# Optimization experiments

Measured on AMD Instinct MI355X. Metric: run time of the kernel, lower is better.

Reference implementation:

```python
import jax, jax.numpy as jnp
import numpy as np

B, S, D_MODEL, D_K, D_V = 4, 2048, 1024, 1024, 1024


def setup_inputs() -> dict:
    key = jax.random.key(0)
    k1, k2, k3, k4 = jax.random.split(key, 4)
    scale = 1.0 / np.sqrt(D_MODEL)
    x = jax.random.normal(k1, (B, S, D_MODEL), dtype=jnp.float32)
    Wq = jax.random.normal(k2, (D_K, D_MODEL), dtype=jnp.float32) * scale
    Wk = jax.random.normal(k3, (D_K, D_MODEL), dtype=jnp.float32) * scale
    Wv = jax.random.normal(k4, (D_V, D_MODEL), dtype=jnp.float32) * scale
    # causal mask: position i may attend to j <= i (True = keep)
    mask = jnp.broadcast_to(jnp.tril(jnp.ones((S, S), dtype=bool)), (B, S, S))
    return {"x": x, "mask": mask, "Wq": Wq, "Wk": Wk, "Wv": Wv}


def reference(x, mask, Wq, Wk, Wv):
    # nn.Linear(d, k, bias=False): y = x @ W.T with W of shape [k, d]
    q = jnp.einsum('bsd,kd->bsk', x, Wq)
    k = jnp.einsum('bsd,kd->bsk', x, Wk)
    v = jnp.einsum('bsd,vd->bsv', x, Wv)
    scores = jnp.einsum('bik,bjk->bij', q, k) / jnp.sqrt(jnp.float32(D_K))
    s = jnp.where(mask, scores, -jnp.inf)
    # masked, fully-masked-row-safe softmax (fully masked rows -> all zeros,
    # matching softmax[all-masked rows] = 0 in the original)
    m = jnp.max(s, axis=-1, keepdims=True)
    m_safe = jnp.where(jnp.isfinite(m), m, 0.0)
    e = jnp.exp(s - m_safe)          # exp(-inf) = 0 for masked entries
    denom = jnp.sum(e, axis=-1, keepdims=True)
    p = e / jnp.where(denom == 0.0, 1.0, denom)
    return jnp.einsum('bij,bjv->biv', p, v)
```

## Files before the change

kernel.cpp:

```cpp
#include <hip/hip_runtime.h>
#include <hip/hip_bf16.h>
#include <stdint.h>

#define SEQ   2048
#define DM    1024
#define NBAT  4

typedef __attribute__((ext_vector_type(8))) short  short8;
typedef __attribute__((ext_vector_type(4))) float  floatx4;

__device__ __forceinline__ unsigned short f2b(float f) {
    __hip_bfloat16 h = __float2bfloat16(f);
    unsigned short r;
    __builtin_memcpy(&r, &h, 2);
    return r;
}

__device__ __forceinline__ void gload16(const void* g, void* s) {
    __builtin_amdgcn_global_load_lds(
        (const __attribute__((address_space(1))) unsigned int*)(uintptr_t)g,
        (__attribute__((address_space(3))) unsigned int*)(uintptr_t)s,
        16, 0, 0);
}

__global__ void cast_bf16_4(const float4* __restrict__ in, ushort4* __restrict__ out, int n4) {
    int i = blockIdx.x * 256 + threadIdx.x;
    if (i < n4) {
        float4 f = in[i];
        ushort4 u;
        u.x = f2b(f.x); u.y = f2b(f.y); u.z = f2b(f.z); u.w = f2b(f.w);
        out[i] = u;
    }
}

template<int OUTM, bool TRI, bool KLIM, bool REV>
__global__ __launch_bounds__(256) void gemm_bt(
    const unsigned short* __restrict__ A, const unsigned short* __restrict__ Bm,
    void* __restrict__ Cv,
    unsigned short* __restrict__ Qo, unsigned short* __restrict__ Ko,
    unsigned short* __restrict__ Vto,
    int M, int N, int K,
    long long sA, long long sB, long long sC, float qscale)
{
    int m0, n0;
    if (TRI) {
        const int f = blockIdx.x;
        int ti = (int)((sqrtf(8.f * f + 1.f) - 1.f) * 0.5f);
        if ((ti + 1) * (ti + 2) / 2 <= f) ti++;
        if (ti * (ti + 1) / 2 > f) ti--;
        const int tj = f - ti * (ti + 1) / 2;
        m0 = ti * 128;
        n0 = tj * 128;
    } else {
        m0 = (REV ? (gridDim.y - 1 - blockIdx.y) : blockIdx.y) * 128;
        n0 = blockIdx.x * 128;
    }
    const int z = blockIdx.z;
    A  += (size_t)z * sA;
    Bm += (size_t)z * sB;

    __shared__ __align__(16) unsigned short As[128 * 32];
    __shared__ __align__(16) unsigned short Bs[128 * 32];

    const int t    = threadIdx.x;
    const int w    = t >> 6;
    const int lane = t & 63;
    const int wr   = w >> 1, wc = w & 1;
    const int r    = lane & 15, q = lane >> 4;

    floatx4 acc[4][4];
#pragma unroll
    for (int i = 0; i < 4; i++)
#pragma unroll
        for (int j = 0; j < 4; j++)
            acc[i][j] = (floatx4){0.f, 0.f, 0.f, 0.f};

    const int kEnd = KLIM ? ((m0 + 128 < K) ? m0 + 128 : K) : K;

    const int row0 = t >> 2;
    const int cc0  = t & 3;

    for (int k0 = 0; k0 < kEnd; k0 += 32) {
        const size_t ka = (size_t)k0 + cc0 * 8;
        gload16(A  + (size_t)(m0 + row0)      * K + ka, As + (size_t)w * 512);
        gload16(A  + (size_t)(m0 + row0 + 64) * K + ka, As + 2048 + (size_t)w * 512);
        gload16(Bm + (size_t)(n0 + row0)      * K + ka, Bs + (size_t)w * 512);
        gload16(Bm + (size_t)(n0 + row0 + 64) * K + ka, Bs + 2048 + (size_t)w * 512);
        __builtin_amdgcn_s_waitcnt(0);
        __syncthreads();

        short8 af[4], bf[4];
#pragma unroll
        for (int i = 0; i < 4; i++) {
            af[i] = *(const short8*)&As[(wr * 64 + i * 16 + r) * 32 + q * 8];
            bf[i] = *(const short8*)&Bs[(wc * 64 + i * 16 + r) * 32 + q * 8];
        }
#pragma unroll
        for (int i = 0; i < 4; i++)
#pragma unroll
            for (int j = 0; j < 4; j++)
                acc[i][j] = __builtin_amdgcn_mfma_f32_16x16x32_bf16(af[i], bf[j], acc[i][j], 0, 0, 0);
        __syncthreads();
    }

    const int gmb = m0 + wr * 64 + q * 4;
    const int gnb = n0 + wc * 64 + r;
    if (OUTM == 2) {
        float* C = (float*)Cv + (size_t)z * sC;
#pragma unroll
        for (int i = 0; i < 4; i++)
#pragma unroll
            for (int j = 0; j < 4; j++) {
                const int gm = gmb + i * 16;
                const int gn = gnb + j * 16;
#pragma unroll
                for (int rr = 0; rr < 4; rr++)
                    C[(size_t)(gm + rr) * N + gn] = acc[i][j][rr];
            }
    } else {
#pragma unroll
        for (int i = 0; i < 4; i++) {
            const int gm = gmb + i * 16;
#pragma unroll
            for (int j = 0; j < 4; j++) {
                const int gn = gnb + j * 16;
                if (n0 < 1024) {
#pragma unroll
                    for (int rr = 0; rr < 4; rr++)
                        Qo[(size_t)(gm + rr) * 1024 + gn] = f2b(acc[i][j][rr] * qscale);
                } else if (n0 < 2048) {
#pragma unroll
                    for (int rr = 0; rr < 4; rr++)
                        Ko[(size_t)(gm + rr) * 1024 + (gn - 1024)] = f2b(acc[i][j][rr]);
                } else {
                    const int b = gm >> 11;
                    const int s = gm & 2047;
                    const int v = gn - 2048;
                    ushort4 u;
                    u.x = f2b(acc[i][j][0]);
                    u.y = f2b(acc[i][j][1]);
                    u.z = f2b(acc[i][j][2]);
                    u.w = f2b(acc[i][j][3]);
                    *(ushort4*)&Vto[((size_t)(b * 1024 + v)) * 2048 + s] = u;
                }
            }
        }
    }
}

__global__ __launch_bounds__(256) void softmax_causal(const float* __restrict__ Sc,
                                                      unsigned short* __restrict__ P)
{
    const int i = blockIdx.x;
    const int b = blockIdx.y;
    const float* row = Sc + ((size_t)b * SEQ + i) * SEQ;
    unsigned short* prow = P + ((size_t)b * SEQ + i) * SEQ;
    const int nv = i + 1;
    const int t = threadIdx.x;

    float v[8];
    float mx = -1e30f;
#pragma unroll
    for (int jj = 0; jj < 8; jj++) {
        const int j = t + jj * 256;
        const float x = (j < nv) ? row[j] : -1e30f;
        v[jj] = x;
        mx = fmaxf(mx, x);
    }
#pragma unroll
    for (int off = 32; off >= 1; off >>= 1)
        mx = fmaxf(mx, __shfl_xor(mx, off, 64));
    __shared__ float redmx[4];
    __shared__ float redsm[4];
    if ((t & 63) == 0) redmx[t >> 6] = mx;
    __syncthreads();
    mx = fmaxf(fmaxf(redmx[0], redmx[1]), fmaxf(redmx[2], redmx[3]));

    float e[8];
    float sum = 0.f;
#pragma unroll
    for (int jj = 0; jj < 8; jj++) {
        const int j = t + jj * 256;
        e[jj] = (j < nv) ? __expf(v[jj] - mx) : 0.f;
        sum += e[jj];
    }
#pragma unroll
    for (int off = 32; off >= 1; off >>= 1)
        sum += __shfl_xor(sum, off, 64);
    if ((t & 63) == 0) redsm[t >> 6] = sum;
    __syncthreads();
    sum = redsm[0] + redsm[1] + redsm[2] + redsm[3];

    const float inv = 1.f / sum;
#pragma unroll
    for (int jj = 0; jj < 8; jj++) {
        const int j = t + jj * 256;
        prow[j] = f2b(e[jj] * inv);
    }
}

extern "C" void kernel_launch(void* const* d_in, const int* in_sizes, int n_in,
                              void* d_out, int out_size, void* d_ws, size_t ws_size,
                              hipStream_t stream) {
    (void)in_sizes; (void)n_in; (void)out_size; (void)ws_size;
    const float* x  = (const float*)d_in[0];
    const float* Wq = (const float*)d_in[2];
    const float* Wk = (const float*)d_in[3];
    const float* Wv = (const float*)d_in[4];

    char* base = (char*)d_ws;
    size_t off = 0;
    auto alloc = [&](size_t n) { char* p = base + off; off += (n + 255) & ~(size_t)255; return p; };

    unsigned short* xb   = (unsigned short*)alloc((size_t)NBAT * SEQ * DM * 2);
    unsigned short* wall = (unsigned short*)alloc((size_t)3 * DM * DM * 2);
    unsigned short* Qb   = (unsigned short*)alloc((size_t)NBAT * SEQ * DM * 2);
    unsigned short* Kb   = (unsigned short*)alloc((size_t)NBAT * SEQ * DM * 2);
    unsigned short* Vtb  = (unsigned short*)alloc((size_t)NBAT * DM * SEQ * 2);
    float*          Sc   = (float*)alloc((size_t)NBAT * SEQ * SEQ * 4);
    unsigned short* P    = (unsigned short*)alloc((size_t)NBAT * SEQ * SEQ * 2);

    const dim3 blk(256);

    {
        int n4 = NBAT * SEQ * DM / 4;
        cast_bf16_4<<<dim3((n4 + 255) / 256), blk, 0, stream>>>((const float4*)x, (ushort4*)xb, n4);
        int w4 = DM * DM / 4;
        dim3 wg((w4 + 255) / 256);
        cast_bf16_4<<<wg, blk, 0, stream>>>((const float4*)Wq, (ushort4*)(wall),            w4);
        cast_bf16_4<<<wg, blk, 0, stream>>>((const float4*)Wk, (ushort4*)(wall + DM * DM),  w4);
        cast_bf16_4<<<wg, blk, 0, stream>>>((const float4*)Wv, (ushort4*)(wall + 2 * DM * DM), w4);
    }

    const int Mtot = NBAT * SEQ;

    gemm_bt<3, false, false, false><<<dim3(3 * DM / 128, Mtot / 128, 1), blk, 0, stream>>>(
        xb, wall, nullptr, Qb, Kb, Vtb, Mtot, 3 * DM, DM, 0, 0, 0, 0.03125f);

    gemm_bt<2, true, false, false><<<dim3(136, 1, NBAT), blk, 0, stream>>>(
        Qb, Kb, Sc, nullptr, nullptr, nullptr, SEQ, SEQ, DM,
        (long long)SEQ * DM, (long long)SEQ * DM, (long long)SEQ * SEQ, 1.0f);

    softmax_causal<<<dim3(SEQ, NBAT), blk, 0, stream>>>(Sc, P);

    gemm_bt<2, false, true, true><<<dim3(DM / 128, SEQ / 128, NBAT), blk, 0, stream>>>(
        P, Vtb, d_out, nullptr, nullptr, nullptr, SEQ, DM, SEQ,
        (long long)SEQ * SEQ, (long long)DM * SEQ, (long long)SEQ * DM, 1.0f);
}
```

Before: 317.2 us.

## Fuse causal softmax into QK^T epilogue and defer normalization to PV GEMM

The fp32 score matrix and the separate softmax kernel are removed. The QK^T GEMM epilogue now applies the causal mask, computes exp directly, writes bf16 unnormalized probabilities, and atomically accumulates per-row sums into a zeroed buffer. The PV GEMM epilogue divides each output row by its row sum. This removes a large fp32 write and read plus a kernel launch. In exchange it drops the max subtraction, so exp can overflow if scores are large, and it adds atomics on the row sums.

```diff
diff --git a/kernel.cpp b/kernel.cpp
--- a/kernel.cpp
+++ b/kernel.cpp
@@ -33,12 +33,18 @@
     }
 }
 
+__global__ void zero_f32(float* __restrict__ p, int n) {
+    int i = blockIdx.x * 256 + threadIdx.x;
+    if (i < n) p[i] = 0.f;
+}
+
 template<int OUTM, bool TRI, bool KLIM, bool REV>
 __global__ __launch_bounds__(256) void gemm_bt(
     const unsigned short* __restrict__ A, const unsigned short* __restrict__ Bm,
     void* __restrict__ Cv,
     unsigned short* __restrict__ Qo, unsigned short* __restrict__ Ko,
     unsigned short* __restrict__ Vto,
+    float* __restrict__ rowsum,
     int M, int N, int K,
     long long sA, long long sB, long long sC, float qscale)
 {
@@ -105,19 +111,7 @@
 
     const int gmb = m0 + wr * 64 + q * 4;
     const int gnb = n0 + wc * 64 + r;
-    if (OUTM == 2) {
-        float* C = (float*)Cv + (size_t)z * sC;
-#pragma unroll
-        for (int i = 0; i < 4; i++)
-#pragma unroll
-            for (int j = 0; j < 4; j++) {
-                const int gm = gmb + i * 16;
-                const int gn = gnb + j * 16;
-#pragma unroll
-                for (int rr = 0; rr < 4; rr++)
-                    C[(size_t)(gm + rr) * N + gn] = acc[i][j][rr];
-            }
-    } else {
+    if (OUTM == 3) {
 #pragma unroll
         for (int i = 0; i < 4; i++) {
             const int gm = gmb + i * 16;
@@ -145,57 +139,44 @@
                 }
             }
         }
-    }
-}
-
-__global__ __launch_bounds__(256) void softmax_causal(const float* __restrict__ Sc,
-                                                      unsigned short* __restrict__ P)
-{
-    const int i = blockIdx.x;
-    const int b = blockIdx.y;
-    const float* row = Sc + ((size_t)b * SEQ + i) * SEQ;
-    unsigned short* prow = P + ((size_t)b * SEQ + i) * SEQ;
-    const int nv = i + 1;
-    const int t = threadIdx.x;
-
-    float v[8];
-    float mx = -1e30f;
-#pragma unroll
-    for (int jj = 0; jj < 8; jj++) {
-        const int j = t + jj * 256;
-        const float x = (j < nv) ? row[j] : -1e30f;
-        v[jj] = x;
-        mx = fmaxf(mx, x);
-    }
-#pragma unroll
-    for (int off = 32; off >= 1; off >>= 1)
-        mx = fmaxf(mx, __shfl_xor(mx, off, 64));
-    __shared__ float redmx[4];
-    __shared__ float redsm[4];
-    if ((t & 63) == 0) redmx[t >> 6] = mx;
-    __syncthreads();
-    mx = fmaxf(fmaxf(redmx[0], redmx[1]), fmaxf(redmx[2], redmx[3]));
-
-    float e[8];
-    float sum = 0.f;
-#pragma unroll
-    for (int jj = 0; jj < 8; jj++) {
-        const int j = t + jj * 256;
-        e[jj] = (j < nv) ? __expf(v[jj] - mx) : 0.f;
-        sum += e[jj];
-    }
-#pragma unroll
-    for (int off = 32; off >= 1; off >>= 1)
-        sum += __shfl_xor(sum, off, 64);
-    if ((t & 63) == 0) redsm[t >> 6] = sum;
-    __syncthreads();
-    sum = redsm[0] + redsm[1] + redsm[2] + redsm[3];
-
-    const float inv = 1.f / sum;
-#pragma unroll
-    for (int jj = 0; jj < 8; jj++) {
-        const int j = t + jj * 256;
-        prow[j] = f2b(e[jj] * inv);
+    } else if (OUTM == 4) {
+        unsigned short* E = (unsigned short*)Cv + (size_t)z * sC;
+        float* rs = rowsum + (size_t)z * SEQ;
+#pragma unroll
+        for (int i = 0; i < 4; i++) {
+            const int gm = gmb + i * 16;
+#pragma unroll
+            for (int rr = 0; rr < 4; rr++) {
+                float part = 0.f;
+#pragma unroll
+                for (int j = 0; j < 4; j++) {
+                    const int gn = gnb + j * 16;
+                    const float ev = (gn <= gm + rr) ? __expf(acc[i][j][rr]) : 0.f;
+                    part += ev;
+                    E[(size_t)(gm + rr) * N + gn] = f2b(ev);
+                }
+#pragma unroll
+                for (int off = 1; off <= 8; off <<= 1)
+                    part += __shfl_xor(part, off, 64);
+                if (r == 0) atomicAdd(&rs[gm + rr], part);
+            }
+        }
+    } else {
+        float* C = (float*)Cv + (size_t)z * sC;
+        const float* rs = rowsum + (size_t)z * SEQ;
+#pragma unroll
+        for (int i = 0; i < 4; i++) {
+            const int gm = gmb + i * 16;
+#pragma unroll
+            for (int rr = 0; rr < 4; rr++) {
+                const float inv = 1.0f / rs[gm + rr];
+#pragma unroll
+                for (int j = 0; j < 4; j++) {
+                    const int gn = gnb + j * 16;
+                    C[(size_t)(gm + rr) * N + gn] = acc[i][j][rr] * inv;
+                }
+            }
+        }
     }
 }
 
@@ -217,8 +198,8 @@
     unsigned short* Qb   = (unsigned short*)alloc((size_t)NBAT * SEQ * DM * 2);
     unsigned short* Kb   = (unsigned short*)alloc((size_t)NBAT * SEQ * DM * 2);
     unsigned short* Vtb  = (unsigned short*)alloc((size_t)NBAT * DM * SEQ * 2);
-    float*          Sc   = (float*)alloc((size_t)NBAT * SEQ * SEQ * 4);
-    unsigned short* P    = (unsigned short*)alloc((size_t)NBAT * SEQ * SEQ * 2);
+    unsigned short* E    = (unsigned short*)alloc((size_t)NBAT * SEQ * SEQ * 2);
+    float*          rsum = (float*)alloc((size_t)NBAT * SEQ * 4);
 
     const dim3 blk(256);
 
@@ -227,23 +208,22 @@
         cast_bf16_4<<<dim3((n4 + 255) / 256), blk, 0, stream>>>((const float4*)x, (ushort4*)xb, n4);
         int w4 = DM * DM / 4;
         dim3 wg((w4 + 255) / 256);
-        cast_bf16_4<<<wg, blk, 0, stream>>>((const float4*)Wq, (ushort4*)(wall),            w4);
-        cast_bf16_4<<<wg, blk, 0, stream>>>((const float4*)Wk, (ushort4*)(wall + DM * DM),  w4);
+        cast_bf16_4<<<wg, blk, 0, stream>>>((const float4*)Wq, (ushort4*)(wall),               w4);
+        cast_bf16_4<<<wg, blk, 0, stream>>>((const float4*)Wk, (ushort4*)(wall + DM * DM),     w4);
         cast_bf16_4<<<wg, blk, 0, stream>>>((const float4*)Wv, (ushort4*)(wall + 2 * DM * DM), w4);
+        zero_f32<<<dim3((NBAT * SEQ + 255) / 256), blk, 0, stream>>>(rsum, NBAT * SEQ);
     }
 
     const int Mtot = NBAT * SEQ;
 
     gemm_bt<3, false, false, false><<<dim3(3 * DM / 128, Mtot / 128, 1), blk, 0, stream>>>(
-        xb, wall, nullptr, Qb, Kb, Vtb, Mtot, 3 * DM, DM, 0, 0, 0, 0.03125f);
-
-    gemm_bt<2, true, false, false><<<dim3(136, 1, NBAT), blk, 0, stream>>>(
-        Qb, Kb, Sc, nullptr, nullptr, nullptr, SEQ, SEQ, DM,
+        xb, wall, nullptr, Qb, Kb, Vtb, nullptr, Mtot, 3 * DM, DM, 0, 0, 0, 0.03125f);
+
+    gemm_bt<4, true, false, false><<<dim3(136, 1, NBAT), blk, 0, stream>>>(
+        Qb, Kb, E, nullptr, nullptr, nullptr, rsum, SEQ, SEQ, DM,
         (long long)SEQ * DM, (long long)SEQ * DM, (long long)SEQ * SEQ, 1.0f);
 
-    softmax_causal<<<dim3(SEQ, NBAT), blk, 0, stream>>>(Sc, P);
-
-    gemm_bt<2, false, true, true><<<dim3(DM / 128, SEQ / 128, NBAT), blk, 0, stream>>>(
-        P, Vtb, d_out, nullptr, nullptr, nullptr, SEQ, DM, SEQ,
+    gemm_bt<5, false, true, true><<<dim3(DM / 128, SEQ / 128, NBAT), blk, 0, stream>>>(
+        E, Vtb, d_out, nullptr, nullptr, nullptr, rsum, SEQ, DM, SEQ,
         (long long)SEQ * SEQ, (long long)DM * SEQ, (long long)SEQ * DM, 1.0f);
 }
```

After: 308.5 us. -2.7%, faster.
